# Kernel optimization log

Measured on AMD Instinct MI355X. Metric: run time of the kernel, lower is better.

The kernel has to match this reference:

```python
import jax, jax.numpy as jnp
import numpy as np

COMMITMENT_COST = 0.25


def setup_inputs() -> dict:
    key = jax.random.key(0)
    k1, k2 = jax.random.split(key)
    inputs = jax.random.normal(k1, (256, 512, 64), dtype=jnp.float32)
    embedding = jax.random.normal(k2, (1024, 64), dtype=jnp.float32) * 4.0
    return {"inputs": inputs, "embedding": embedding}


def reference(inputs, embedding):
    # inputs: [B, T, D], embedding: [K, D]
    input_shape = inputs.shape
    D = embedding.shape[-1]
    flat = inputs.reshape(-1, D)  # [N, D]
    # squared-L2 distances: [N, K]
    distances = (
        jnp.sum(flat * flat, axis=1, keepdims=True)
        + jnp.sum(embedding * embedding, axis=1)[None, :]
        - 2.0 * flat @ embedding.T
    )
    encoding_indices = jnp.argmin(distances, axis=1)  # [N]
    # one-hot @ embedding == gather
    quantized = embedding[encoding_indices].reshape(input_shape)  # [B, T, D]
    # squared-L2 commitment / codebook loss
    e_latent_loss = jnp.sum((jax.lax.stop_gradient(quantized) - inputs) ** 2, axis=-1)
    q_latent_loss = jnp.sum((quantized - jax.lax.stop_gradient(inputs)) ** 2, axis=-1)
    quantization_loss = q_latent_loss + COMMITMENT_COST * e_latent_loss  # [B, T]
    # straight-through estimator
    quantized_sg = inputs + jax.lax.stop_gradient(quantized - inputs)
    encoding_indices = encoding_indices.reshape(input_shape[:-1])  # [B, T]
    return quantized_sg, encoding_indices, quantization_loss
```

## Files before the change

kernel.cpp:

```cpp
#include <hip/hip_runtime.h>
#include <hip/hip_bf16.h>

#define D 64
#define KCODES 1024
#define MARGIN 0.25f
#define FLAG_CAP 8192

typedef __attribute__((ext_vector_type(8))) short bf16x8;
typedef __attribute__((ext_vector_type(4))) float f32x4;

__device__ inline unsigned short f2bf(float f) {
    union { __hip_bfloat16 h; unsigned short s; } cv;
    cv.h = __float2bfloat16(f);
    return cv.s;
}
__device__ inline float bf2f(unsigned short v) {
    union { unsigned short s; __hip_bfloat16 h; } cv;
    cv.s = v;
    return __bfloat162float(cv.h);
}

__global__ __launch_bounds__(256) void prep_kernel(
    const float* __restrict__ emb, float* __restrict__ e2,
    unsigned short* __restrict__ ehi, unsigned short* __restrict__ elo,
    unsigned int* __restrict__ counter) {
    int t = blockIdx.x * 256 + threadIdx.x;
    if (t == 0) *counter = 0u;
    if (t < KCODES) {
        const float4* ep = (const float4*)(emb + (size_t)t * D);
        float s0 = 0.f, s1 = 0.f, s2 = 0.f, s3 = 0.f;
#pragma unroll
        for (int i = 0; i < 16; ++i) {
            float4 v = ep[i];
            s0 = fmaf(v.x, v.x, s0);
            s1 = fmaf(v.y, v.y, s1);
            s2 = fmaf(v.z, v.z, s2);
            s3 = fmaf(v.w, v.w, s3);
        }
        e2[t] = (s0 + s1) + (s2 + s3);
    }
    float v = emb[t];
    unsigned short h = f2bf(v);
    ehi[t] = h;
    elo[t] = f2bf(v - bf2f(h));
}

__global__ __launch_bounds__(256) void vq_mfma_kernel(
    const float* __restrict__ x, const float* __restrict__ emb,
    const float* __restrict__ e2, const unsigned short* __restrict__ ehi,
    const unsigned short* __restrict__ elo, float* __restrict__ out_q,
    float* __restrict__ out_idx, float* __restrict__ out_loss,
    unsigned int* __restrict__ counter, int* __restrict__ flaglist) {
    __shared__ int s_bi[256];
    const int tid = threadIdx.x;
    const int lane = tid & 63;
    const int wave = __builtin_amdgcn_readfirstlane(tid >> 6);
    const int quad = lane >> 4;
    const int l15 = lane & 15;
    const int rowBase = blockIdx.x * 256 + wave * 64;

    bf16x8 ah[4][2], al[4][2];
#pragma unroll
    for (int rs = 0; rs < 4; ++rs) {
        const float* xr = x + (size_t)(rowBase + rs * 16 + l15) * D;
#pragma unroll
        for (int c = 0; c < 2; ++c) {
            const float4* p = (const float4*)(xr + c * 32 + quad * 8);
            float4 f0 = p[0], f1 = p[1];
            float f[8] = {f0.x, f0.y, f0.z, f0.w, f1.x, f1.y, f1.z, f1.w};
            bf16x8 h, l;
#pragma unroll
            for (int j = 0; j < 8; ++j) {
                unsigned short hu = f2bf(f[j]);
                h[j] = (short)hu;
                l[j] = (short)f2bf(f[j] - bf2f(hu));
            }
            ah[rs][c] = h;
            al[rs][c] = l;
        }
    }

    float m1[4][4], m2[4][4];
    int i1[4][4];
#pragma unroll
    for (int rs = 0; rs < 4; ++rs)
#pragma unroll
        for (int r = 0; r < 4; ++r) {
            m1[rs][r] = 3.4e38f;
            m2[rs][r] = 3.4e38f;
            i1[rs][r] = 0;
        }

    for (int t = 0; t < 64; ++t) {
        const int code = t * 16 + l15;
        const float e2v = e2[code];
        const unsigned short* hb = ehi + (size_t)code * D + quad * 8;
        const unsigned short* lb = elo + (size_t)code * D + quad * 8;
        bf16x8 bh0 = *(const bf16x8*)(hb);
        bf16x8 bh1 = *(const bf16x8*)(hb + 32);
        bf16x8 bl0 = *(const bf16x8*)(lb);
        bf16x8 bl1 = *(const bf16x8*)(lb + 32);
#pragma unroll
        for (int rs = 0; rs < 4; ++rs) {
            f32x4 acc = {0.f, 0.f, 0.f, 0.f};
            acc = __builtin_amdgcn_mfma_f32_16x16x32_bf16(ah[rs][0], bh0, acc, 0, 0, 0);
            acc = __builtin_amdgcn_mfma_f32_16x16x32_bf16(ah[rs][0], bl0, acc, 0, 0, 0);
            acc = __builtin_amdgcn_mfma_f32_16x16x32_bf16(al[rs][0], bh0, acc, 0, 0, 0);
            acc = __builtin_amdgcn_mfma_f32_16x16x32_bf16(ah[rs][1], bh1, acc, 0, 0, 0);
            acc = __builtin_amdgcn_mfma_f32_16x16x32_bf16(ah[rs][1], bl1, acc, 0, 0, 0);
            acc = __builtin_amdgcn_mfma_f32_16x16x32_bf16(al[rs][1], bh1, acc, 0, 0, 0);
#pragma unroll
            for (int r = 0; r < 4; ++r) {
                float v = fmaf(-2.0f, acc[r], e2v);
                if (v < m1[rs][r]) {
                    m2[rs][r] = m1[rs][r];
                    m1[rs][r] = v;
                    i1[rs][r] = code;
                } else {
                    m2[rs][r] = fminf(m2[rs][r], v);
                }
            }
        }
    }

#pragma unroll
    for (int rs = 0; rs < 4; ++rs)
#pragma unroll
        for (int r = 0; r < 4; ++r) {
            float v1 = m1[rs][r], v2 = m2[rs][r];
            int ix = i1[rs][r];
#pragma unroll
            for (int mask = 1; mask < 16; mask <<= 1) {
                float o1 = __shfl_xor(v1, mask);
                int oi = __shfl_xor(ix, mask);
                float o2 = __shfl_xor(v2, mask);
                v2 = fminf(fminf(v2, o2), fmaxf(v1, o1));
                bool take = (o1 < v1) || (o1 == v1 && oi < ix);
                v1 = take ? o1 : v1;
                ix = take ? oi : ix;
            }
            m1[rs][r] = v1;
            m2[rs][r] = v2;
            i1[rs][r] = ix;
        }

    if (l15 == 0) {
#pragma unroll
        for (int rs = 0; rs < 4; ++rs)
#pragma unroll
            for (int r = 0; r < 4; ++r) {
                int lrow = wave * 64 + rs * 16 + quad * 4 + r;
                s_bi[lrow] = i1[rs][r];
                if (m2[rs][r] - m1[rs][r] < MARGIN) {
                    unsigned int slot = atomicAdd(counter, 1u);
                    if (slot < FLAG_CAP) flaglist[slot] = blockIdx.x * 256 + lrow;
                }
            }
    }
    __syncthreads();

    {
        const int row = blockIdx.x * 256 + tid;
        const int bi = s_bi[tid];
        const float4* qp = (const float4*)(emb + (size_t)bi * D);
        const float4* xp = (const float4*)(x + (size_t)row * D);
        float4* oq = (float4*)(out_q + (size_t)row * D);
        float l0 = 0.f, l1 = 0.f, l2 = 0.f, l3 = 0.f;
#pragma unroll
        for (int i = 0; i < 16; ++i) {
            float4 q = qp[i];
            float4 xv = xp[i];
            float a0 = q.x - xv.x, a1 = q.y - xv.y, a2 = q.z - xv.z, a3 = q.w - xv.w;
            l0 = fmaf(a0, a0, l0);
            l1 = fmaf(a1, a1, l1);
            l2 = fmaf(a2, a2, l2);
            l3 = fmaf(a3, a3, l3);
            float4 o;
            o.x = xv.x + a0;
            o.y = xv.y + a1;
            o.z = xv.z + a2;
            o.w = xv.w + a3;
            oq[i] = o;
        }
        float s = (l0 + l1) + (l2 + l3);
        out_idx[row] = (float)bi;
        out_loss[row] = s + 0.25f * s;
    }
}

__global__ __launch_bounds__(256) void rescore_kernel(
    const float* __restrict__ x, const float* __restrict__ emb,
    const float* __restrict__ e2, float* __restrict__ out_q,
    float* __restrict__ out_idx, float* __restrict__ out_loss,
    const unsigned int* __restrict__ counter, const int* __restrict__ flaglist) {
    __shared__ float s_d[256];
    __shared__ int s_i[256];
    __shared__ float s_a[D];
    unsigned int n = *counter;
    if (n > FLAG_CAP) n = FLAG_CAP;
    const int tid = threadIdx.x;
    for (unsigned int f = blockIdx.x; f < n; f += gridDim.x) {
        const int row = flaglist[f];
        const float* xr = x + (size_t)row * D;
        float xv[D];
        const float4* xp = (const float4*)xr;
#pragma unroll
        for (int i = 0; i < 16; ++i) {
            float4 v = xp[i];
            xv[4 * i + 0] = v.x;
            xv[4 * i + 1] = v.y;
            xv[4 * i + 2] = v.z;
            xv[4 * i + 3] = v.w;
        }
        float bd = 3.4e38f;
        int bi = 0;
        for (int kk = 0; kk < 4; ++kk) {
            const int k = tid + kk * 256;
            const float* ek = emb + (size_t)k * D;
            float d0 = 0.f, d1 = 0.f, d2 = 0.f, d3 = 0.f;
#pragma unroll
            for (int i = 0; i < 16; ++i) {
                d0 = fmaf(xv[4 * i + 0], ek[4 * i + 0], d0);
                d1 = fmaf(xv[4 * i + 1], ek[4 * i + 1], d1);
                d2 = fmaf(xv[4 * i + 2], ek[4 * i + 2], d2);
                d3 = fmaf(xv[4 * i + 3], ek[4 * i + 3], d3);
            }
            float dist = fmaf(-2.0f, (d0 + d1) + (d2 + d3), e2[k]);
            if (dist < bd) { bd = dist; bi = k; }
        }
        s_d[tid] = bd;
        s_i[tid] = bi;
        __syncthreads();
        for (int s = 128; s > 0; s >>= 1) {
            if (tid < s) {
                float od = s_d[tid + s];
                int oi = s_i[tid + s];
                if (od < s_d[tid] || (od == s_d[tid] && oi < s_i[tid])) {
                    s_d[tid] = od;
                    s_i[tid] = oi;
                }
            }
            __syncthreads();
        }
        const int fbi = s_i[0];
        if (tid < D) {
            float xe = xr[tid];
            float a = emb[(size_t)fbi * D + tid] - xe;
            out_q[(size_t)row * D + tid] = xe + a;
            s_a[tid] = a * a;
        }
        __syncthreads();
        if (tid == 0) {
            float l0 = 0.f, l1 = 0.f, l2 = 0.f, l3 = 0.f;
            for (int i = 0; i < 16; ++i) {
                l0 += s_a[4 * i + 0];
                l1 += s_a[4 * i + 1];
                l2 += s_a[4 * i + 2];
                l3 += s_a[4 * i + 3];
            }
            float s = (l0 + l1) + (l2 + l3);
            out_loss[row] = s + 0.25f * s;
            out_idx[row] = (float)fbi;
        }
        __syncthreads();
    }
}

extern "C" void kernel_launch(void* const* d_in, const int* in_sizes, int n_in,
                              void* d_out, int out_size, void* d_ws, size_t ws_size,
                              hipStream_t stream) {
    const float* x = (const float*)d_in[0];
    const float* emb = (const float*)d_in[1];
    const int nrows = in_sizes[0] / D;

    float* out_q = (float*)d_out;
    float* out_idx = out_q + (size_t)nrows * D;
    float* out_loss = out_idx + nrows;

    char* ws = (char*)d_ws;
    float* e2 = (float*)ws;
    unsigned short* ehi = (unsigned short*)(ws + 4096);
    unsigned short* elo = (unsigned short*)(ws + 4096 + 131072);
    unsigned int* counter = (unsigned int*)(ws + 4096 + 2 * 131072);
    int* flaglist = (int*)(ws + 4096 + 2 * 131072 + 64);

    prep_kernel<<<(KCODES * D) / 256, 256, 0, stream>>>(emb, e2, ehi, elo, counter);
    vq_mfma_kernel<<<nrows / 256, 256, 0, stream>>>(x, emb, e2, ehi, elo, out_q,
                                                    out_idx, out_loss, counter,
                                                    flaglist);
    rescore_kernel<<<256, 256, 0, stream>>>(x, emb, e2, out_q, out_idx, out_loss,
                                            counter, flaglist);
}
```

Measured before the change: 193.5 us.

## Use single fp16 MFMA pass with in-block rescoring of near-tie rows

Replaces the split-bf16 three-product MFMA distance computation with a single fp16 product per k-chunk, widening the tie margin to absorb the larger error. Rows whose best and second-best distances fall within the margin are rescored in exact fp32 inside the same block, so the separate rescore kernel, global counter and flag list go away. It also halves rows per block, prefetches the next codebook tile into registers, and makes the argmin update branchless. The risk is that many rows fall inside the wider margin, since each flagged row stalls its whole block in a serialized fp32 rescore with several barriers. fp16 also limits range, though these inputs fit.

Result: slower. 552.4 us (+185.4%).

```diff
diff --git a/kernel.cpp b/kernel.cpp
--- a/kernel.cpp
+++ b/kernel.cpp
@@ -1,31 +1,19 @@
 #include <hip/hip_runtime.h>
-#include <hip/hip_bf16.h>
 
 #define D 64
 #define KCODES 1024
-#define MARGIN 0.25f
-#define FLAG_CAP 8192
-
-typedef __attribute__((ext_vector_type(8))) short bf16x8;
-typedef __attribute__((ext_vector_type(4))) float f32x4;
-
-__device__ inline unsigned short f2bf(float f) {
-    union { __hip_bfloat16 h; unsigned short s; } cv;
-    cv.h = __float2bfloat16(f);
-    return cv.s;
-}
-__device__ inline float bf2f(unsigned short v) {
-    union { unsigned short s; __hip_bfloat16 h; } cv;
-    cv.s = v;
-    return __bfloat162float(cv.h);
-}
-
-__global__ __launch_bounds__(256) void prep_kernel(
-    const float* __restrict__ emb, float* __restrict__ e2,
-    unsigned short* __restrict__ ehi, unsigned short* __restrict__ elo,
-    unsigned int* __restrict__ counter) {
+#define MARGIN 1.5f
+
+typedef _Float16 f16x8 __attribute__((ext_vector_type(8)));
+typedef float f32x4 __attribute__((ext_vector_type(4)));
+
+#define WS_E2 0
+#define WS_EHF 8192
+
+__global__ __launch_bounds__(256) void prep_kernel(const float* __restrict__ emb,
+                                                   float* __restrict__ e2,
+                                                   _Float16* __restrict__ ehf) {
     int t = blockIdx.x * 256 + threadIdx.x;
-    if (t == 0) *counter = 0u;
     if (t < KCODES) {
         const float4* ep = (const float4*)(emb + (size_t)t * D);
         float s0 = 0.f, s1 = 0.f, s2 = 0.f, s3 = 0.f;
@@ -39,51 +27,51 @@
         }
         e2[t] = (s0 + s1) + (s2 + s3);
     }
-    float v = emb[t];
-    unsigned short h = f2bf(v);
-    ehi[t] = h;
-    elo[t] = f2bf(v - bf2f(h));
+    if (t < 16) e2[KCODES + t] = 0.f;
+    ehf[t] = (_Float16)emb[t];
 }
 
-__global__ __launch_bounds__(256) void vq_mfma_kernel(
+__global__ __launch_bounds__(256, 4) void vq_kernel(
     const float* __restrict__ x, const float* __restrict__ emb,
-    const float* __restrict__ e2, const unsigned short* __restrict__ ehi,
-    const unsigned short* __restrict__ elo, float* __restrict__ out_q,
-    float* __restrict__ out_idx, float* __restrict__ out_loss,
-    unsigned int* __restrict__ counter, int* __restrict__ flaglist) {
-    __shared__ int s_bi[256];
+    const float* __restrict__ e2, const _Float16* __restrict__ ehf,
+    float* __restrict__ out_q, float* __restrict__ out_idx,
+    float* __restrict__ out_loss) {
+    __shared__ int s_bi[128];
+    __shared__ int s_flag[128];
+    __shared__ int s_nflag;
+    __shared__ float s_d[256];
+    __shared__ int s_i[256];
+
     const int tid = threadIdx.x;
     const int lane = tid & 63;
     const int wave = __builtin_amdgcn_readfirstlane(tid >> 6);
     const int quad = lane >> 4;
     const int l15 = lane & 15;
-    const int rowBase = blockIdx.x * 256 + wave * 64;
-
-    bf16x8 ah[4][2], al[4][2];
-#pragma unroll
-    for (int rs = 0; rs < 4; ++rs) {
+    const int rowBase = blockIdx.x * 128 + wave * 32;
+
+    if (tid == 0) s_nflag = 0;
+
+    f16x8 a[2][2];
+#pragma unroll
+    for (int rs = 0; rs < 2; ++rs) {
         const float* xr = x + (size_t)(rowBase + rs * 16 + l15) * D;
 #pragma unroll
         for (int c = 0; c < 2; ++c) {
             const float4* p = (const float4*)(xr + c * 32 + quad * 8);
             float4 f0 = p[0], f1 = p[1];
-            float f[8] = {f0.x, f0.y, f0.z, f0.w, f1.x, f1.y, f1.z, f1.w};
-            bf16x8 h, l;
-#pragma unroll
-            for (int j = 0; j < 8; ++j) {
-                unsigned short hu = f2bf(f[j]);
-                h[j] = (short)hu;
-                l[j] = (short)f2bf(f[j] - bf2f(hu));
-            }
-            ah[rs][c] = h;
-            al[rs][c] = l;
-        }
-    }
-
-    float m1[4][4], m2[4][4];
-    int i1[4][4];
-#pragma unroll
-    for (int rs = 0; rs < 4; ++rs)
+            f16x8 h;
+            h[0] = (_Float16)f0.x; h[1] = (_Float16)f0.y;
+            h[2] = (_Float16)f0.z; h[3] = (_Float16)f0.w;
+            h[4] = (_Float16)f1.x; h[5] = (_Float16)f1.y;
+            h[6] = (_Float16)f1.z; h[7] = (_Float16)f1.w;
+            a[rs][c] = h;
+        }
+    }
+
+    float m1[2][4], m2[2][4];
+    int i1[2][4];
+#pragma unroll
+    for (int rs = 0; rs < 2; ++rs)
 #pragma unroll
         for (int r = 0; r < 4; ++r) {
             m1[rs][r] = 3.4e38f;
@@ -91,40 +79,36 @@
             i1[rs][r] = 0;
         }
 
+    const _Float16* bbase = ehf + (size_t)l15 * D + quad * 8;
+    f16x8 nb0 = *(const f16x8*)(bbase);
+    f16x8 nb1 = *(const f16x8*)(bbase + 32);
+    float ne2 = e2[l15];
     for (int t = 0; t < 64; ++t) {
-        const int code = t * 16 + l15;
-        const float e2v = e2[code];
-        const unsigned short* hb = ehi + (size_t)code * D + quad * 8;
-        const unsigned short* lb = elo + (size_t)code * D + quad * 8;
-        bf16x8 bh0 = *(const bf16x8*)(hb);
-        bf16x8 bh1 = *(const bf16x8*)(hb + 32);
-        bf16x8 bl0 = *(const bf16x8*)(lb);
-        bf16x8 bl1 = *(const bf16x8*)(lb + 32);
-#pragma unroll
-        for (int rs = 0; rs < 4; ++rs) {
+        f16x8 b0 = nb0, b1 = nb1;
+        float e2v = ne2;
+        const _Float16* nb = bbase + (size_t)(t + 1) * 16 * D;
+        nb0 = *(const f16x8*)(nb);
+        nb1 = *(const f16x8*)(nb + 32);
+        ne2 = e2[(t + 1) * 16 + l15];
+        const int code = (t << 4) + l15;
+#pragma unroll
+        for (int rs = 0; rs < 2; ++rs) {
             f32x4 acc = {0.f, 0.f, 0.f, 0.f};
-            acc = __builtin_amdgcn_mfma_f32_16x16x32_bf16(ah[rs][0], bh0, acc, 0, 0, 0);
-            acc = __builtin_amdgcn_mfma_f32_16x16x32_bf16(ah[rs][0], bl0, acc, 0, 0, 0);
-            acc = __builtin_amdgcn_mfma_f32_16x16x32_bf16(al[rs][0], bh0, acc, 0, 0, 0);
-            acc = __builtin_amdgcn_mfma_f32_16x16x32_bf16(ah[rs][1], bh1, acc, 0, 0, 0);
-            acc = __builtin_amdgcn_mfma_f32_16x16x32_bf16(ah[rs][1], bl1, acc, 0, 0, 0);
-            acc = __builtin_amdgcn_mfma_f32_16x16x32_bf16(al[rs][1], bh1, acc, 0, 0, 0);
+            acc = __builtin_amdgcn_mfma_f32_16x16x32_f16(a[rs][0], b0, acc, 0, 0, 0);
+            acc = __builtin_amdgcn_mfma_f32_16x16x32_f16(a[rs][1], b1, acc, 0, 0, 0);
 #pragma unroll
             for (int r = 0; r < 4; ++r) {
                 float v = fmaf(-2.0f, acc[r], e2v);
-                if (v < m1[rs][r]) {
-                    m2[rs][r] = m1[rs][r];
-                    m1[rs][r] = v;
-                    i1[rs][r] = code;
-                } else {
-                    m2[rs][r] = fminf(m2[rs][r], v);
-                }
-            }
-        }
-    }
-
-#pragma unroll
-    for (int rs = 0; rs < 4; ++rs)
+                bool take = v < m1[rs][r];
+                i1[rs][r] = take ? code : i1[rs][r];
+                m2[rs][r] = fminf(m2[rs][r], fmaxf(m1[rs][r], v));
+                m1[rs][r] = fminf(m1[rs][r], v);
+            }
+        }
+    }
+
+#pragma unroll
+    for (int rs = 0; rs < 2; ++rs)
 #pragma unroll
         for (int r = 0; r < 4; ++r) {
             float v1 = m1[rs][r], v2 = m2[rs][r];
@@ -146,21 +130,70 @@
 
     if (l15 == 0) {
 #pragma unroll
-        for (int rs = 0; rs < 4; ++rs)
+        for (int rs = 0; rs < 2; ++rs)
 #pragma unroll
             for (int r = 0; r < 4; ++r) {
-                int lrow = wave * 64 + rs * 16 + quad * 4 + r;
+                int lrow = wave * 32 + rs * 16 + quad * 4 + r;
                 s_bi[lrow] = i1[rs][r];
                 if (m2[rs][r] - m1[rs][r] < MARGIN) {
-                    unsigned int slot = atomicAdd(counter, 1u);
-                    if (slot < FLAG_CAP) flaglist[slot] = blockIdx.x * 256 + lrow;
+                    int slot = atomicAdd(&s_nflag, 1);
+                    s_flag[slot] = lrow;
                 }
             }
     }
     __syncthreads();
 
-    {
-        const int row = blockIdx.x * 256 + tid;
+    const int nf = s_nflag;
+    for (int f = 0; f < nf; ++f) {
+        const int lrow = s_flag[f];
+        const int row = blockIdx.x * 128 + lrow;
+        const float* xr = x + (size_t)row * D;
+        float xv[D];
+        const float4* xp = (const float4*)xr;
+#pragma unroll
+        for (int i = 0; i < 16; ++i) {
+            float4 v = xp[i];
+            xv[4 * i + 0] = v.x;
+            xv[4 * i + 1] = v.y;
+            xv[4 * i + 2] = v.z;
+            xv[4 * i + 3] = v.w;
+        }
+        float bd = 3.4e38f;
+        int bi = 0;
+        for (int kk = 0; kk < 4; ++kk) {
+            const int k = tid + kk * 256;
+            const float* ek = emb + (size_t)k * D;
+            float d0 = 0.f, d1 = 0.f, d2 = 0.f, d3 = 0.f;
+#pragma unroll
+            for (int i = 0; i < 16; ++i) {
+                d0 = fmaf(xv[4 * i + 0], ek[4 * i + 0], d0);
+                d1 = fmaf(xv[4 * i + 1], ek[4 * i + 1], d1);
+                d2 = fmaf(xv[4 * i + 2], ek[4 * i + 2], d2);
+                d3 = fmaf(xv[4 * i + 3], ek[4 * i + 3], d3);
+            }
+            float dist = fmaf(-2.0f, (d0 + d1) + (d2 + d3), e2[k]);
+            if (dist < bd) { bd = dist; bi = k; }
+        }
+        s_d[tid] = bd;
+        s_i[tid] = bi;
+        __syncthreads();
+        for (int s = 128; s > 0; s >>= 1) {
+            if (tid < s) {
+                float od = s_d[tid + s];
+                int oi = s_i[tid + s];
+                if (od < s_d[tid] || (od == s_d[tid] && oi < s_i[tid])) {
+                    s_d[tid] = od;
+                    s_i[tid] = oi;
+                }
+            }
+            __syncthreads();
+        }
+        if (tid == 0) s_bi[lrow] = s_i[0];
+        __syncthreads();
+    }
+
+    if (tid < 128) {
+        const int row = blockIdx.x * 128 + tid;
         const int bi = s_bi[tid];
         const float4* qp = (const float4*)(emb + (size_t)bi * D);
         const float4* xp = (const float4*)(x + (size_t)row * D);
@@ -188,84 +221,6 @@
     }
 }
 
-__global__ __launch_bounds__(256) void rescore_kernel(
-    const float* __restrict__ x, const float* __restrict__ emb,
-    const float* __restrict__ e2, float* __restrict__ out_q,
-    float* __restrict__ out_idx, float* __restrict__ out_loss,
-    const unsigned int* __restrict__ counter, const int* __restrict__ flaglist) {
-    __shared__ float s_d[256];
-    __shared__ int s_i[256];
-    __shared__ float s_a[D];
-    unsigned int n = *counter;
-    if (n > FLAG_CAP) n = FLAG_CAP;
-    const int tid = threadIdx.x;
-    for (unsigned int f = blockIdx.x; f < n; f += gridDim.x) {
-        const int row = flaglist[f];
-        const float* xr = x + (size_t)row * D;
-        float xv[D];
-        const float4* xp = (const float4*)xr;
-#pragma unroll
-        for (int i = 0; i < 16; ++i) {
-            float4 v = xp[i];
-            xv[4 * i + 0] = v.x;
-            xv[4 * i + 1] = v.y;
-            xv[4 * i + 2] = v.z;
-            xv[4 * i + 3] = v.w;
-        }
-        float bd = 3.4e38f;
-        int bi = 0;
-        for (int kk = 0; kk < 4; ++kk) {
-            const int k = tid + kk * 256;
-            const float* ek = emb + (size_t)k * D;
-            float d0 = 0.f, d1 = 0.f, d2 = 0.f, d3 = 0.f;
-#pragma unroll
-            for (int i = 0; i < 16; ++i) {
-                d0 = fmaf(xv[4 * i + 0], ek[4 * i + 0], d0);
-                d1 = fmaf(xv[4 * i + 1], ek[4 * i + 1], d1);
-                d2 = fmaf(xv[4 * i + 2], ek[4 * i + 2], d2);
-                d3 = fmaf(xv[4 * i + 3], ek[4 * i + 3], d3);
-            }
-            float dist = fmaf(-2.0f, (d0 + d1) + (d2 + d3), e2[k]);
-            if (dist < bd) { bd = dist; bi = k; }
-        }
-        s_d[tid] = bd;
-        s_i[tid] = bi;
-        __syncthreads();
-        for (int s = 128; s > 0; s >>= 1) {
-            if (tid < s) {
-                float od = s_d[tid + s];
-                int oi = s_i[tid + s];
-                if (od < s_d[tid] || (od == s_d[tid] && oi < s_i[tid])) {
-                    s_d[tid] = od;
-                    s_i[tid] = oi;
-                }
-            }
-            __syncthreads();
-        }
-        const int fbi = s_i[0];
-        if (tid < D) {
-            float xe = xr[tid];
-            float a = emb[(size_t)fbi * D + tid] - xe;
-            out_q[(size_t)row * D + tid] = xe + a;
-            s_a[tid] = a * a;
-        }
-        __syncthreads();
-        if (tid == 0) {
-            float l0 = 0.f, l1 = 0.f, l2 = 0.f, l3 = 0.f;
-            for (int i = 0; i < 16; ++i) {
-                l0 += s_a[4 * i + 0];
-                l1 += s_a[4 * i + 1];
-                l2 += s_a[4 * i + 2];
-                l3 += s_a[4 * i + 3];
-            }
-            float s = (l0 + l1) + (l2 + l3);
-            out_loss[row] = s + 0.25f * s;
-            out_idx[row] = (float)fbi;
-        }
-        __syncthreads();
-    }
-}
-
 extern "C" void kernel_launch(void* const* d_in, const int* in_sizes, int n_in,
                               void* d_out, int out_size, void* d_ws, size_t ws_size,
                               hipStream_t stream) {
@@ -278,16 +233,10 @@
     float* out_loss = out_idx + nrows;
 
     char* ws = (char*)d_ws;
-    float* e2 = (float*)ws;
-    unsigned short* ehi = (unsigned short*)(ws + 4096);
-    unsigned short* elo = (unsigned short*)(ws + 4096 + 131072);
-    unsigned int* counter = (unsigned int*)(ws + 4096 + 2 * 131072);
-    int* flaglist = (int*)(ws + 4096 + 2 * 131072 + 64);
-
-    prep_kernel<<<(KCODES * D) / 256, 256, 0, stream>>>(emb, e2, ehi, elo, counter);
-    vq_mfma_kernel<<<nrows / 256, 256, 0, stream>>>(x, emb, e2, ehi, elo, out_q,
-                                                    out_idx, out_loss, counter,
-                                                    flaglist);
-    rescore_kernel<<<256, 256, 0, stream>>>(x, emb, e2, out_q, out_idx, out_loss,
-                                            counter, flaglist);
+    float* e2 = (float*)(ws + WS_E2);
+    _Float16* ehf = (_Float16*)(ws + WS_EHF);
+
+    prep_kernel<<<(KCODES * D) / 256, 256, 0, stream>>>(emb, e2, ehf);
+    vq_kernel<<<nrows / 128, 256, 0, stream>>>(x, emb, e2, ehf, out_q, out_idx,
+                                               out_loss);
 }
```
